# Performance work log

Measured on AMD Instinct MI355X. Metric: run time of the kernel, lower is better.

## Reference

```python
import jax, jax.numpy as jnp
import numpy as np

LN_EPS = 1e-5
BN_EPS = 1e-5
ATTN_EPS = 1e-6

def _ln(x, g, b):
    m = x.mean(-1, keepdims=True)
    v = x.var(-1, keepdims=True)
    return (x - m) / jnp.sqrt(v + LN_EPS) * g + b

def setup_inputs() -> dict:
    key = jax.random.key(0)
    ks = jax.random.split(key, 16)
    B, C, N = 4, 256, 8192
    s = 0.05
    def rn(k, shape, scale=1.0):
        return jax.random.normal(k, shape, jnp.float32) * scale
    return {
        "x1": rn(ks[0], (B, C, N)),
        "x2": rn(ks[1], (B, C, N)),
        "Wq": rn(ks[2], (C, C), s), "bq": rn(ks[3], (C,), s),
        "Wk": rn(ks[4], (C, C), s), "bk": rn(ks[5], (C,), s),
        "Wv": rn(ks[6], (C, C), s), "bv": rn(ks[7], (C,), s),
        "threshold": jnp.array([0.1], jnp.float32),
        "W1": rn(ks[8], (2 * C, 2 * C), s),
        "W2": rn(ks[9], (C, 2 * C), s),
        "g1": jnp.ones((C,), jnp.float32), "b1": jnp.zeros((C,), jnp.float32),
        "g2": jnp.ones((C,), jnp.float32), "b2": jnp.zeros((C,), jnp.float32),
        "Wa": rn(ks[10], (C, C), s), "ba": rn(ks[11], (C,), s),
        "bn_g": jnp.ones((C,), jnp.float32), "bn_b": jnp.zeros((C,), jnp.float32),
        "bn_m": jnp.zeros((C,), jnp.float32), "bn_v": jnp.ones((C,), jnp.float32),
    }

def reference(x1, x2, Wq, bq, Wk, bk, Wv, bv, threshold, W1, W2,
              g1, b1, g2, b2, Wa, ba, bn_g, bn_b, bn_m, bn_v):
    B, C, N = x1.shape
    H = 4
    d = C // H
    def conv1x1(x, W, b):  # nn.Conv1d(C, C, 1): [B,C,N] -> [B,C,N]
        return jnp.einsum('bcn,oc->bon', x, W) + b[:, None]
    # projections -> [B, N, H, d]
    q = conv1x1(x1, Wq, bq).transpose(0, 2, 1).reshape(B, N, H, d)
    k = conv1x1(x2, Wk, bk).transpose(0, 2, 1).reshape(B, N, H, d)
    v = conv1x1(x2, Wv, bv).transpose(0, 2, 1).reshape(B, N, H, d)
    # DynamicSparseLinearAttention
    Q = jax.nn.elu(q) + 1.0
    K = jax.nn.elu(k) + 1.0
    S = v.shape[1]
    vals = v / S
    KV = jnp.einsum('nshd,nshv->nhdv', K, vals)               # [B,H,d,d]
    scores = jnp.einsum('nlhd,nhd->nlh', Q, K.sum(axis=1))    # [B,N,H]
    sparse = jnp.where(scores > threshold[0], scores, 0.0)
    Z = 1.0 / (sparse + ATTN_EPS)
    msg = jnp.einsum('nlhd,nhdv,nlh->nlhv', Q, KV, Z) * S     # [B,N,H,d]
    # view [B,N,C]; the transpose(1,2).transpose(1,2) in torch cancels
    msg = msg.reshape(B, N, H * d)
    msg = _ln(msg, g1, b1)
    msg = jnp.concatenate([x1.transpose(0, 2, 1), msg], axis=2)  # [B,N,2C]
    msg = jax.nn.relu(msg @ W1.T) @ W2.T                         # [B,N,C]
    msg = _ln(msg, g2, b2).transpose(0, 2, 1)                    # [B,C,N]
    # aug shortcut: conv1x1 + BatchNorm1d (eval mode, running stats)
    aug = conv1x1(x1, Wa, ba)
    aug = (aug - bn_m[None, :, None]) / jnp.sqrt(bn_v[None, :, None] + BN_EPS)
    aug = aug * bn_g[None, :, None] + bn_b[None, :, None]
    return msg + x1 + aug
```

## Files before the change

kernel.cpp:

```cpp
#include <hip/hip_runtime.h>

#define BB 4
#define CC 256
#define NN 8192
#define HH 4
#define NCH 16

typedef unsigned short u16;
typedef __bf16 bf16x8 __attribute__((ext_vector_type(8)));
typedef float f32x4 __attribute__((ext_vector_type(4)));

__device__ __forceinline__ float bf2f(unsigned u) {
  return __uint_as_float(u << 16);
}
__device__ __forceinline__ u16 f2bf(float f) {
  unsigned u = __float_as_uint(f);
  return (u16)((u + 0x7fffu + ((u >> 16) & 1u)) >> 16);
}
__device__ __forceinline__ void bf8_to_f32(uint4 r, float* f) {
  f[0] = __uint_as_float(r.x << 16); f[1] = __uint_as_float(r.x & 0xffff0000u);
  f[2] = __uint_as_float(r.y << 16); f[3] = __uint_as_float(r.y & 0xffff0000u);
  f[4] = __uint_as_float(r.z << 16); f[5] = __uint_as_float(r.z & 0xffff0000u);
  f[6] = __uint_as_float(r.w << 16); f[7] = __uint_as_float(r.w & 0xffff0000u);
}

__global__ __launch_bounds__(256) void cvt_all_kernel(
    const float* __restrict__ wq, const float* __restrict__ wk,
    const float* __restrict__ wv, const float* __restrict__ wa,
    const float* __restrict__ w1, const float* __restrict__ w2,
    u16* __restrict__ oq, u16* __restrict__ ok, u16* __restrict__ ov,
    u16* __restrict__ oa, u16* __restrict__ o1, u16* __restrict__ o2) {
  int i = blockIdx.x * 256 + threadIdx.x;
  const float* src;
  u16* dst;
  int off;
  if (i < 65536) { src = wq; dst = oq; off = i; }
  else if (i < 131072) { src = wk; dst = ok; off = i - 65536; }
  else if (i < 196608) { src = wv; dst = ov; off = i - 131072; }
  else if (i < 262144) { src = wa; dst = oa; off = i - 196608; }
  else if (i < 524288) { src = w1; dst = o1; off = i - 262144; }
  else { src = w2; dst = o2; off = i - 524288; }
  dst[off] = f2bf(src[off]);
}

__global__ __launch_bounds__(256) void transpose_kernel(const float* __restrict__ x1,
                                                        const float* __restrict__ x2,
                                                        u16* __restrict__ x1t,
                                                        u16* __restrict__ x2t) {
  __shared__ float T[64][65];
  const int bz = blockIdx.z;
  const int b = bz & 3;
  const float* x = (bz < 4) ? x1 : x2;
  u16* xt = (bz < 4) ? x1t : x2t;
  const int c0 = blockIdx.y * 64, n0 = blockIdx.x * 64;
  const float* xp = x + ((size_t)b * CC + c0) * NN + n0;
#pragma unroll
  for (int it = 0; it < 4; ++it) {
    int idx = threadIdx.x + it * 256;
    int r = idx >> 4, seg = idx & 15;
    float4 v = *(const float4*)(xp + (size_t)r * NN + seg * 4);
    T[r][seg * 4 + 0] = v.x; T[r][seg * 4 + 1] = v.y;
    T[r][seg * 4 + 2] = v.z; T[r][seg * 4 + 3] = v.w;
  }
  __syncthreads();
  u16* op = xt + ((size_t)b * NN + n0) * CC + c0;
  const int j = threadIdx.x >> 2, g = threadIdx.x & 3;
#pragma unroll
  for (int i = 0; i < 4; ++i) {
    int c = g * 16 + i * 4;
    uint2 pk;
    pk.x = (unsigned)f2bf(T[c + 0][j]) | ((unsigned)f2bf(T[c + 1][j]) << 16);
    pk.y = (unsigned)f2bf(T[c + 2][j]) | ((unsigned)f2bf(T[c + 3][j]) << 16);
    *(uint2*)(op + (size_t)j * CC + c) = pk;
  }
}

template <int MODE>
__global__ __launch_bounds__(256) void gemm_kernel(
    const u16* __restrict__ A1, const u16* __restrict__ A2,
    const u16* __restrict__ W, const float* __restrict__ bias,
    const float* __restrict__ e0, const float* __restrict__ e1,
    const float* __restrict__ e2, const float* __restrict__ e3,
    u16* __restrict__ outp, int K, int O) {
  __shared__ u16 As[128][72];
  __shared__ u16 Ws[128][72];
  const int m0 = blockIdx.x * 128, o0 = blockIdx.y * 128;
  const int tid = threadIdx.x, lane = tid & 63, wave = tid >> 6;
  const int wm = (wave >> 1) * 64, wo = (wave & 1) * 64;
  const int fr = lane & 15, fq = lane >> 4;
  f32x4 acc[4][4] = {};
  const int nkt = K >> 6;
  for (int kt = 0; kt < nkt; ++kt) {
    const int k0 = kt << 6;
    const u16* Ap;
    int rsA;
    if (MODE == 4) {
      Ap = (k0 < 256) ? (A1 + k0) : (A2 + (k0 - 256));
      rsA = 256;
    } else {
      Ap = A1 + k0;
      rsA = K;
    }
    const u16* Wp = W + k0;
#pragma unroll
    for (int i = 0; i < 4; ++i) {
      int idx = tid + i * 256;
      int r = idx >> 3, s = idx & 7;
      *(uint4*)(&As[r][s * 8]) = *(const uint4*)(Ap + (size_t)(m0 + r) * rsA + s * 8);
      *(uint4*)(&Ws[r][s * 8]) = *(const uint4*)(Wp + (size_t)(o0 + r) * K + s * 8);
    }
    __syncthreads();
#pragma unroll
    for (int kk = 0; kk < 2; ++kk) {
      bf16x8 af[4], bfr[4];
#pragma unroll
      for (int mi = 0; mi < 4; ++mi)
        af[mi] = __builtin_bit_cast(bf16x8, *(const uint4*)(&As[wm + mi * 16 + fr][kk * 32 + fq * 8]));
#pragma unroll
      for (int oi = 0; oi < 4; ++oi)
        bfr[oi] = __builtin_bit_cast(bf16x8, *(const uint4*)(&Ws[wo + oi * 16 + fr][kk * 32 + fq * 8]));
#pragma unroll
      for (int mi = 0; mi < 4; ++mi)
#pragma unroll
        for (int oi = 0; oi < 4; ++oi)
          acc[mi][oi] = __builtin_amdgcn_mfma_f32_16x16x32_bf16(af[mi], bfr[oi], acc[mi][oi], 0, 0, 0);
    }
    __syncthreads();
  }
  const int bb_ = m0 >> 13;
  const int nb = m0 & (NN - 1);
#pragma unroll
  for (int oi = 0; oi < 4; ++oi) {
    const int col = o0 + wo + oi * 16 + fr;
    float b0 = 0.f, sc = 1.f, sh = 0.f;
    if (MODE == 0 || MODE == 1 || MODE == 2) b0 = bias[col];
    if (MODE == 3) {
      sc = e0[col] * rsqrtf(e3[col] + 1e-5f);
      sh = (bias[col] - e2[col]) * sc + e1[col];
    }
#pragma unroll
    for (int mi = 0; mi < 4; ++mi) {
      const int rowb = m0 + wm + mi * 16 + fq * 4;
      if (MODE == 1 || MODE == 2) {
        float v[4];
#pragma unroll
        for (int r = 0; r < 4; ++r) {
          float t = acc[mi][oi][r] + b0;
          if (MODE == 1) t = (t > 0.f) ? (t + 1.f) : __expf(t);
          v[r] = t;
        }
        uint2 pk;
        pk.x = (unsigned)f2bf(v[0]) | ((unsigned)f2bf(v[1]) << 16);
        pk.y = (unsigned)f2bf(v[2]) | ((unsigned)f2bf(v[3]) << 16);
        const int nloc = nb + wm + mi * 16 + fq * 4;
        *(uint2*)(outp + ((size_t)bb_ * CC + col) * NN + nloc) = pk;
      } else {
#pragma unroll
        for (int r = 0; r < 4; ++r) {
          float v = acc[mi][oi][r];
          if (MODE == 0) {
            v += b0;
            v = (v > 0.f) ? (v + 1.f) : __expf(v);
          } else if (MODE == 3) {
            v = v * sc + sh;
          } else if (MODE == 4) {
            v = fmaxf(v, 0.f);
          }
          outp[(size_t)(rowb + r) * O + col] = f2bf(v);
        }
      }
    }
  }
}

__global__ __launch_bounds__(256) void ksum_kernel(const u16* __restrict__ K2,
                                                   float* __restrict__ Ksum) {
  __shared__ float red[4];
  const int b = blockIdx.y, c = blockIdx.x, tid = threadIdx.x;
  const u16* p = K2 + ((size_t)b * CC + c) * NN;
  float acc = 0.f;
#pragma unroll
  for (int j = 0; j < 4; ++j) {
    uint4 raw = *(const uint4*)(p + (j * 256 + tid) * 8);
    float f[8];
    bf8_to_f32(raw, f);
#pragma unroll
    for (int q = 0; q < 8; ++q) acc += f[q];
  }
#pragma unroll
  for (int m = 1; m < 64; m <<= 1) acc += __shfl_xor(acc, m);
  if ((tid & 63) == 0) red[tid >> 6] = acc;
  __syncthreads();
  if (tid == 0) Ksum[b * CC + c] = red[0] + red[1] + red[2] + red[3];
}

__global__ __launch_bounds__(256) void kvpartial_kernel(const u16* __restrict__ K2,
                                                        const u16* __restrict__ V2,
                                                        float* __restrict__ Pkv) {
  __shared__ u16 Ks[64][72];
  __shared__ u16 Vs[64][72];
  const int b = blockIdx.z, h = blockIdx.y, ch = blockIdx.x;
  const int tid = threadIdx.x, lane = tid & 63, w = tid >> 6;
  const int fr = lane & 15, fq = lane >> 4;
  const size_t base = ((size_t)b * CC + h * 64) * NN + (size_t)ch * (NN / NCH);
  f32x4 acc[4] = {};
  for (int step = 0; step < (NN / NCH) / 64; ++step) {
#pragma unroll
    for (int i = 0; i < 2; ++i) {
      int r = (tid >> 3) + i * 32, s = tid & 7;
      *(uint4*)(&Ks[r][s * 8]) = *(const uint4*)(K2 + base + (size_t)r * NN + step * 64 + s * 8);
      *(uint4*)(&Vs[r][s * 8]) = *(const uint4*)(V2 + base + (size_t)r * NN + step * 64 + s * 8);
    }
    __syncthreads();
#pragma unroll
    for (int kk = 0; kk < 2; ++kk) {
      bf16x8 af = __builtin_bit_cast(bf16x8, *(const uint4*)(&Ks[w * 16 + fr][kk * 32 + fq * 8]));
#pragma unroll
      for (int oi = 0; oi < 4; ++oi) {
        bf16x8 bfr = __builtin_bit_cast(bf16x8, *(const uint4*)(&Vs[oi * 16 + fr][kk * 32 + fq * 8]));
        acc[oi] = __builtin_amdgcn_mfma_f32_16x16x32_bf16(af, bfr, acc[oi], 0, 0, 0);
      }
    }
    __syncthreads();
  }
  float* o = Pkv + (((size_t)ch * (BB * HH) + b * HH + h) << 12);
#pragma unroll
  for (int oi = 0; oi < 4; ++oi)
#pragma unroll
    for (int r = 0; r < 4; ++r)
      o[(w * 16 + fq * 4 + r) * 64 + oi * 16 + fr] = acc[oi][r];
}

__global__ __launch_bounds__(256) void kvreduce_kernel(const float* __restrict__ Pkv,
                                                       u16* __restrict__ KVT) {
  int i = blockIdx.x * 256 + threadIdx.x;
  int bh = i >> 12, dk = (i >> 6) & 63, dv = i & 63;
  float s = 0.f;
#pragma unroll
  for (int ch = 0; ch < NCH; ++ch)
    s += Pkv[(((size_t)ch * (BB * HH) + bh) << 12) + (dk << 6) + dv];
  KVT[((size_t)bh << 12) + (dv << 6) + dk] = f2bf(s);
}

__global__ __launch_bounds__(256) void score_kernel(const u16* __restrict__ Qt,
                                                    const float* __restrict__ Ksum,
                                                    const float* __restrict__ thrp,
                                                    float* __restrict__ Zbuf) {
  int gid = blockIdx.x * 256 + threadIdx.x;
  int b = gid >> 13;
  const u16* qp = Qt + (size_t)gid * CC;
  const float* ks = Ksum + b * CC;
  float acc[HH] = {0.f, 0.f, 0.f, 0.f};
  for (int c8 = 0; c8 < 32; ++c8) {
    uint4 raw = *(const uint4*)(qp + c8 * 8);
    float f[8];
    bf8_to_f32(raw, f);
    float s = 0.f;
#pragma unroll
    for (int j = 0; j < 8; ++j) s += f[j] * ks[c8 * 8 + j];
    acc[c8 >> 3] += s;
  }
  float thr = thrp[0];
  float4 z;
  z.x = 1.f / (((acc[0] > thr) ? acc[0] : 0.f) + 1e-6f);
  z.y = 1.f / (((acc[1] > thr) ? acc[1] : 0.f) + 1e-6f);
  z.z = 1.f / (((acc[2] > thr) ? acc[2] : 0.f) + 1e-6f);
  z.w = 1.f / (((acc[3] > thr) ? acc[3] : 0.f) + 1e-6f);
  *(float4*)(Zbuf + (size_t)gid * 4) = z;
}

__global__ __launch_bounds__(256) void msggemm_kernel(const u16* __restrict__ Qt,
                                                      const u16* __restrict__ KVT,
                                                      const float* __restrict__ Zbuf,
                                                      u16* __restrict__ msgout) {
  __shared__ u16 As[128][72];
  __shared__ u16 Ws[64][72];
  const int m0 = blockIdx.x * 128, h = blockIdx.y, b = blockIdx.z;
  const int tid = threadIdx.x, lane = tid & 63, wave = tid >> 6;
  const int wm = (wave >> 1) * 64, wo = (wave & 1) * 32;
  const int fr = lane & 15, fq = lane >> 4;
  const u16* Ap = Qt + ((size_t)b * NN + m0) * CC + h * 64;
#pragma unroll
  for (int i = 0; i < 4; ++i) {
    int idx = tid + i * 256;
    int r = idx >> 3, s = idx & 7;
    *(uint4*)(&As[r][s * 8]) = *(const uint4*)(Ap + (size_t)r * CC + s * 8);
  }
  const u16* Wp = KVT + (((size_t)b * HH + h) << 12);
#pragma unroll
  for (int i = 0; i < 2; ++i) {
    int idx = tid + i * 256;
    int r = idx >> 3, s = idx & 7;
    *(uint4*)(&Ws[r][s * 8]) = *(const uint4*)(Wp + (size_t)r * 64 + s * 8);
  }
  __syncthreads();
  f32x4 acc[4][2] = {};
#pragma unroll
  for (int kk = 0; kk < 2; ++kk) {
    bf16x8 af[4], bfr[2];
#pragma unroll
    for (int mi = 0; mi < 4; ++mi)
      af[mi] = __builtin_bit_cast(bf16x8, *(const uint4*)(&As[wm + mi * 16 + fr][kk * 32 + fq * 8]));
#pragma unroll
    for (int oi = 0; oi < 2; ++oi)
      bfr[oi] = __builtin_bit_cast(bf16x8, *(const uint4*)(&Ws[wo + oi * 16 + fr][kk * 32 + fq * 8]));
#pragma unroll
    for (int mi = 0; mi < 4; ++mi)
#pragma unroll
      for (int oi = 0; oi < 2; ++oi)
        acc[mi][oi] = __builtin_amdgcn_mfma_f32_16x16x32_bf16(af[mi], bfr[oi], acc[mi][oi], 0, 0, 0);
  }
#pragma unroll
  for (int oi = 0; oi < 2; ++oi) {
    const int col = h * 64 + wo + oi * 16 + fr;
#pragma unroll
    for (int mi = 0; mi < 4; ++mi) {
      const int rowb = m0 + wm + mi * 16 + fq * 4;
#pragma unroll
      for (int r = 0; r < 4; ++r) {
        const int row = rowb + r;
        float z = Zbuf[((size_t)b * NN + row) * HH + h];
        msgout[((size_t)b * NN + row) * CC + col] = f2bf(acc[mi][oi][r] * z);
      }
    }
  }
}

template <bool AUG>
__global__ __launch_bounds__(256) void ln_kernel(const u16* __restrict__ in,
                                                 u16* __restrict__ outb,
                                                 const float* __restrict__ g,
                                                 const float* __restrict__ bb,
                                                 const u16* __restrict__ aug) {
  const int tid = threadIdx.x, lane = tid & 63, w = tid >> 6;
  const size_t row0 = (size_t)blockIdx.x * 32;
  float gv[4], bv[4];
#pragma unroll
  for (int q = 0; q < 4; ++q) {
    gv[q] = g[lane + 64 * q];
    bv[q] = bb[lane + 64 * q];
  }
  for (int i = 0; i < 8; ++i) {
    const size_t row = row0 + i * 4 + w;
    const u16* p = in + row * CC;
    float v[4], s1 = 0.f, s2 = 0.f;
#pragma unroll
    for (int q = 0; q < 4; ++q) {
      v[q] = bf2f(p[lane + 64 * q]);
      s1 += v[q];
      s2 += v[q] * v[q];
    }
#pragma unroll
    for (int m = 1; m < 64; m <<= 1) {
      s1 += __shfl_xor(s1, m);
      s2 += __shfl_xor(s2, m);
    }
    const float mean = s1 * (1.f / CC);
    const float var = s2 * (1.f / CC) - mean * mean;
    const float rs = rsqrtf(var + 1e-5f);
    u16* o = outb + row * CC;
#pragma unroll
    for (int q = 0; q < 4; ++q) {
      float ov = (v[q] - mean) * rs * gv[q] + bv[q];
      if (AUG) ov += bf2f(aug[row * CC + lane + 64 * q]);
      o[lane + 64 * q] = f2bf(ov);
    }
  }
}

__global__ __launch_bounds__(256) void addout_kernel(const u16* __restrict__ tv,
                                                     const float* __restrict__ x1,
                                                     float* __restrict__ outp) {
  __shared__ float T[64][65];
  const int b = blockIdx.z, c0 = blockIdx.y * 64, n0 = blockIdx.x * 64;
  const u16* tp = tv + ((size_t)b * NN + n0) * CC + c0;
#pragma unroll
  for (int i = 0; i < 2; ++i) {
    int idx = threadIdx.x + i * 256;
    int r = idx >> 3, s = idx & 7;
    uint4 raw = *(const uint4*)(tp + (size_t)r * CC + s * 8);
    float f[8];
    bf8_to_f32(raw, f);
#pragma unroll
    for (int j = 0; j < 8; ++j) T[s * 8 + j][r] = f[j];
  }
  __syncthreads();
  const float* xp = x1 + ((size_t)b * CC + c0) * NN + n0;
  float* op = outp + ((size_t)b * CC + c0) * NN + n0;
#pragma unroll
  for (int i = 0; i < 16; ++i) {
    int idx = threadIdx.x + i * 256;
    int c = idx >> 6, j = idx & 63;
    op[(size_t)c * NN + j] = T[c][j] + xp[(size_t)c * NN + j];
  }
}

extern "C" void kernel_launch(void* const* d_in, const int* in_sizes, int n_in,
                              void* d_out, int out_size, void* d_ws, size_t ws_size,
                              hipStream_t stream) {
  (void)in_sizes; (void)n_in; (void)out_size; (void)ws_size;
  const float* x1 = (const float*)d_in[0];
  const float* x2 = (const float*)d_in[1];
  const float* Wq = (const float*)d_in[2];
  const float* bq = (const float*)d_in[3];
  const float* Wk = (const float*)d_in[4];
  const float* bk = (const float*)d_in[5];
  const float* Wv = (const float*)d_in[6];
  const float* bv = (const float*)d_in[7];
  const float* thr = (const float*)d_in[8];
  const float* W1 = (const float*)d_in[9];
  const float* W2 = (const float*)d_in[10];
  const float* g1 = (const float*)d_in[11];
  const float* b1 = (const float*)d_in[12];
  const float* g2 = (const float*)d_in[13];
  const float* b2 = (const float*)d_in[14];
  const float* Wa = (const float*)d_in[15];
  const float* ba = (const float*)d_in[16];
  const float* bng = (const float*)d_in[17];
  const float* bnb = (const float*)d_in[18];
  const float* bnm = (const float*)d_in[19];
  const float* bnv = (const float*)d_in[20];
  float* out = (float*)d_out;

  char* ws = (char*)d_ws;
  constexpr size_t SZ = (size_t)BB * NN * CC * sizeof(u16);
  u16* x1t = (u16*)(ws);
  u16* x2t = (u16*)(ws + SZ);
  u16* Qt = (u16*)(ws + 2 * SZ);
  u16* K2 = (u16*)(ws + 3 * SZ);
  u16* V2 = (u16*)(ws + 4 * SZ);
  u16* augt = (u16*)(ws + 5 * SZ);
  u16* msgout = (u16*)(ws + 6 * SZ);
  u16* h1 = Qt;
  u16* mlp2 = x2t;
  u16* msgN = V2;
  u16* tv = V2;
  float* Pkv = (float*)msgout;
  char* tail = ws + 7 * SZ;
  float* Ksum = (float*)tail;
  float* Zbuf = (float*)(tail + 4096);
  u16* KVT = (u16*)(tail + 4096 + 524288);
  u16* Wqb = (u16*)(tail + 4096 + 524288 + 131072);
  u16* Wkb = Wqb + CC * CC;
  u16* Wvb = Wkb + CC * CC;
  u16* Wab = Wvb + CC * CC;
  u16* W1b = Wab + CC * CC;
  u16* W2b = W1b + 512 * 512;

  cvt_all_kernel<<<dim3(2560), 256, 0, stream>>>(Wq, Wk, Wv, Wa, W1, W2,
                                                 Wqb, Wkb, Wvb, Wab, W1b, W2b);

  transpose_kernel<<<dim3(NN / 64, CC / 64, 2 * BB), 256, 0, stream>>>(x1, x2, x1t, x2t);

  gemm_kernel<0><<<dim3(256, 2), 256, 0, stream>>>(x1t, nullptr, Wqb, bq, nullptr, nullptr, nullptr, nullptr, Qt, 256, 256);
  gemm_kernel<1><<<dim3(256, 2), 256, 0, stream>>>(x2t, nullptr, Wkb, bk, nullptr, nullptr, nullptr, nullptr, K2, 256, 256);
  gemm_kernel<2><<<dim3(256, 2), 256, 0, stream>>>(x2t, nullptr, Wvb, bv, nullptr, nullptr, nullptr, nullptr, V2, 256, 256);
  gemm_kernel<3><<<dim3(256, 2), 256, 0, stream>>>(x1t, nullptr, Wab, ba, bng, bnb, bnm, bnv, augt, 256, 256);

  ksum_kernel<<<dim3(CC, BB), 256, 0, stream>>>(K2, Ksum);
  kvpartial_kernel<<<dim3(NCH, HH, BB), 256, 0, stream>>>(K2, V2, Pkv);
  kvreduce_kernel<<<dim3(256), 256, 0, stream>>>(Pkv, KVT);
  score_kernel<<<dim3(128), 256, 0, stream>>>(Qt, Ksum, thr, Zbuf);
  msggemm_kernel<<<dim3(NN / 128, HH, BB), 256, 0, stream>>>(Qt, KVT, Zbuf, msgout);
  ln_kernel<false><<<dim3(1024), 256, 0, stream>>>(msgout, msgN, g1, b1, nullptr);

  gemm_kernel<4><<<dim3(256, 4), 256, 0, stream>>>(x1t, msgN, W1b, nullptr, nullptr, nullptr, nullptr, nullptr, h1, 512, 512);
  gemm_kernel<5><<<dim3(256, 2), 256, 0, stream>>>(h1, nullptr, W2b, nullptr, nullptr, nullptr, nullptr, nullptr, mlp2, 512, 256);

  ln_kernel<true><<<dim3(1024), 256, 0, stream>>>(mlp2, tv, g2, b2, augt);
  addout_kernel<<<dim3(NN / 64, CC / 64, BB), 256, 0, stream>>>(tv, x1, out);
}
```

Measured before the change: 187.5 us.

## Use direct global-to-LDS loads, fuse score into msggemm, vectorize layernorm

GEMM and KV-partial tiles are now loaded straight from global memory into LDS with global_load_lds, and the padded LDS rows are dropped so the direct-load layout fits. The score/Z computation moves into the message GEMM, which computes it from the Q tile already staged in LDS, removing one launch and the Zbuf round trip. LayerNorm now reads and writes four contiguous bf16 values per lane instead of strided scalar accesses. Removing the row padding may bring back LDS bank conflicts on the MFMA fragment reads.

Measured after the change: 192.1 us. 2.4% more time.

```diff
diff --git a/kernel.cpp b/kernel.cpp
--- a/kernel.cpp
+++ b/kernel.cpp
@@ -22,6 +22,15 @@
   f[2] = __uint_as_float(r.y << 16); f[3] = __uint_as_float(r.y & 0xffff0000u);
   f[4] = __uint_as_float(r.z << 16); f[5] = __uint_as_float(r.z & 0xffff0000u);
   f[6] = __uint_as_float(r.w << 16); f[7] = __uint_as_float(r.w & 0xffff0000u);
+}
+__device__ __forceinline__ void bf4_to_f32(uint2 r, float* f) {
+  f[0] = __uint_as_float(r.x << 16); f[1] = __uint_as_float(r.x & 0xffff0000u);
+  f[2] = __uint_as_float(r.y << 16); f[3] = __uint_as_float(r.y & 0xffff0000u);
+}
+__device__ __forceinline__ void gload16(const u16* g, u16* l) {
+  __builtin_amdgcn_global_load_lds(
+      (const __attribute__((address_space(1))) unsigned int*)g,
+      (__attribute__((address_space(3))) unsigned int*)l, 16, 0, 0);
 }
 
 __global__ __launch_bounds__(256) void cvt_all_kernel(
@@ -82,8 +91,8 @@
     const float* __restrict__ e0, const float* __restrict__ e1,
     const float* __restrict__ e2, const float* __restrict__ e3,
     u16* __restrict__ outp, int K, int O) {
-  __shared__ u16 As[128][72];
-  __shared__ u16 Ws[128][72];
+  __shared__ u16 As[128 * 64];
+  __shared__ u16 Ws[128 * 64];
   const int m0 = blockIdx.x * 128, o0 = blockIdx.y * 128;
   const int tid = threadIdx.x, lane = tid & 63, wave = tid >> 6;
   const int wm = (wave >> 1) * 64, wo = (wave & 1) * 64;
@@ -105,9 +114,9 @@
 #pragma unroll
     for (int i = 0; i < 4; ++i) {
       int idx = tid + i * 256;
-      int r = idx >> 3, s = idx & 7;
-      *(uint4*)(&As[r][s * 8]) = *(const uint4*)(Ap + (size_t)(m0 + r) * rsA + s * 8);
-      *(uint4*)(&Ws[r][s * 8]) = *(const uint4*)(Wp + (size_t)(o0 + r) * K + s * 8);
+      int rr = idx >> 3, ss = idx & 7;
+      gload16(Ap + (size_t)(m0 + rr) * rsA + ss * 8, &As[(i * 256 + wave * 64) * 8]);
+      gload16(Wp + (size_t)(o0 + rr) * K + ss * 8, &Ws[(i * 256 + wave * 64) * 8]);
     }
     __syncthreads();
 #pragma unroll
@@ -115,10 +124,10 @@
       bf16x8 af[4], bfr[4];
 #pragma unroll
       for (int mi = 0; mi < 4; ++mi)
-        af[mi] = __builtin_bit_cast(bf16x8, *(const uint4*)(&As[wm + mi * 16 + fr][kk * 32 + fq * 8]));
+        af[mi] = __builtin_bit_cast(bf16x8, *(const uint4*)(&As[(wm + mi * 16 + fr) * 64 + kk * 32 + fq * 8]));
 #pragma unroll
       for (int oi = 0; oi < 4; ++oi)
-        bfr[oi] = __builtin_bit_cast(bf16x8, *(const uint4*)(&Ws[wo + oi * 16 + fr][kk * 32 + fq * 8]));
+        bfr[oi] = __builtin_bit_cast(bf16x8, *(const uint4*)(&Ws[(wo + oi * 16 + fr) * 64 + kk * 32 + fq * 8]));
 #pragma unroll
       for (int mi = 0; mi < 4; ++mi)
 #pragma unroll
@@ -197,8 +206,8 @@
 __global__ __launch_bounds__(256) void kvpartial_kernel(const u16* __restrict__ K2,
                                                         const u16* __restrict__ V2,
                                                         float* __restrict__ Pkv) {
-  __shared__ u16 Ks[64][72];
-  __shared__ u16 Vs[64][72];
+  __shared__ u16 Ks[64 * 64];
+  __shared__ u16 Vs[64 * 64];
   const int b = blockIdx.z, h = blockIdx.y, ch = blockIdx.x;
   const int tid = threadIdx.x, lane = tid & 63, w = tid >> 6;
   const int fr = lane & 15, fq = lane >> 4;
@@ -207,17 +216,18 @@
   for (int step = 0; step < (NN / NCH) / 64; ++step) {
 #pragma unroll
     for (int i = 0; i < 2; ++i) {
-      int r = (tid >> 3) + i * 32, s = tid & 7;
-      *(uint4*)(&Ks[r][s * 8]) = *(const uint4*)(K2 + base + (size_t)r * NN + step * 64 + s * 8);
-      *(uint4*)(&Vs[r][s * 8]) = *(const uint4*)(V2 + base + (size_t)r * NN + step * 64 + s * 8);
+      int idx = tid + i * 256;
+      int rr = idx >> 3, ss = idx & 7;
+      gload16(K2 + base + (size_t)rr * NN + step * 64 + ss * 8, &Ks[(i * 256 + w * 64) * 8]);
+      gload16(V2 + base + (size_t)rr * NN + step * 64 + ss * 8, &Vs[(i * 256 + w * 64) * 8]);
     }
     __syncthreads();
 #pragma unroll
     for (int kk = 0; kk < 2; ++kk) {
-      bf16x8 af = __builtin_bit_cast(bf16x8, *(const uint4*)(&Ks[w * 16 + fr][kk * 32 + fq * 8]));
+      bf16x8 af = __builtin_bit_cast(bf16x8, *(const uint4*)(&Ks[(w * 16 + fr) * 64 + kk * 32 + fq * 8]));
 #pragma unroll
       for (int oi = 0; oi < 4; ++oi) {
-        bf16x8 bfr = __builtin_bit_cast(bf16x8, *(const uint4*)(&Vs[oi * 16 + fr][kk * 32 + fq * 8]));
+        bf16x8 bfr = __builtin_bit_cast(bf16x8, *(const uint4*)(&Vs[(oi * 16 + fr) * 64 + kk * 32 + fq * 8]));
         acc[oi] = __builtin_amdgcn_mfma_f32_16x16x32_bf16(af, bfr, acc[oi], 0, 0, 0);
       }
     }
@@ -242,85 +252,76 @@
   KVT[((size_t)bh << 12) + (dv << 6) + dk] = f2bf(s);
 }
 
-__global__ __launch_bounds__(256) void score_kernel(const u16* __restrict__ Qt,
-                                                    const float* __restrict__ Ksum,
-                                                    const float* __restrict__ thrp,
-                                                    float* __restrict__ Zbuf) {
-  int gid = blockIdx.x * 256 + threadIdx.x;
-  int b = gid >> 13;
-  const u16* qp = Qt + (size_t)gid * CC;
-  const float* ks = Ksum + b * CC;
-  float acc[HH] = {0.f, 0.f, 0.f, 0.f};
-  for (int c8 = 0; c8 < 32; ++c8) {
-    uint4 raw = *(const uint4*)(qp + c8 * 8);
-    float f[8];
-    bf8_to_f32(raw, f);
-    float s = 0.f;
-#pragma unroll
-    for (int j = 0; j < 8; ++j) s += f[j] * ks[c8 * 8 + j];
-    acc[c8 >> 3] += s;
-  }
-  float thr = thrp[0];
-  float4 z;
-  z.x = 1.f / (((acc[0] > thr) ? acc[0] : 0.f) + 1e-6f);
-  z.y = 1.f / (((acc[1] > thr) ? acc[1] : 0.f) + 1e-6f);
-  z.z = 1.f / (((acc[2] > thr) ? acc[2] : 0.f) + 1e-6f);
-  z.w = 1.f / (((acc[3] > thr) ? acc[3] : 0.f) + 1e-6f);
-  *(float4*)(Zbuf + (size_t)gid * 4) = z;
-}
-
 __global__ __launch_bounds__(256) void msggemm_kernel(const u16* __restrict__ Qt,
                                                       const u16* __restrict__ KVT,
-                                                      const float* __restrict__ Zbuf,
+                                                      const float* __restrict__ Ksum,
+                                                      const float* __restrict__ thrp,
                                                       u16* __restrict__ msgout) {
-  __shared__ u16 As[128][72];
-  __shared__ u16 Ws[64][72];
+  __shared__ u16 As[128 * 64];
+  __shared__ u16 Ws[64 * 64];
+  __shared__ float Zs[128];
   const int m0 = blockIdx.x * 128, h = blockIdx.y, b = blockIdx.z;
   const int tid = threadIdx.x, lane = tid & 63, wave = tid >> 6;
   const int wm = (wave >> 1) * 64, wo = (wave & 1) * 32;
   const int fr = lane & 15, fq = lane >> 4;
+  const float thrv = thrp[0];
   const u16* Ap = Qt + ((size_t)b * NN + m0) * CC + h * 64;
 #pragma unroll
   for (int i = 0; i < 4; ++i) {
     int idx = tid + i * 256;
-    int r = idx >> 3, s = idx & 7;
-    *(uint4*)(&As[r][s * 8]) = *(const uint4*)(Ap + (size_t)r * CC + s * 8);
+    int rr = idx >> 3, ss = idx & 7;
+    gload16(Ap + (size_t)rr * CC + ss * 8, &As[(i * 256 + wave * 64) * 8]);
   }
   const u16* Wp = KVT + (((size_t)b * HH + h) << 12);
 #pragma unroll
   for (int i = 0; i < 2; ++i) {
     int idx = tid + i * 256;
-    int r = idx >> 3, s = idx & 7;
-    *(uint4*)(&Ws[r][s * 8]) = *(const uint4*)(Wp + (size_t)r * 64 + s * 8);
+    int rr = idx >> 3, ss = idx & 7;
+    gload16(Wp + (size_t)rr * 64 + ss * 8, &Ws[(i * 256 + wave * 64) * 8]);
   }
   __syncthreads();
+  {
+    const int row = tid >> 1, half = tid & 1;
+    const float* ksh = Ksum + b * CC + h * 64 + half * 32;
+    float za = 0.f;
+#pragma unroll
+    for (int j8 = 0; j8 < 4; ++j8) {
+      uint4 raw = *(const uint4*)(&As[row * 64 + half * 32 + j8 * 8]);
+      float f[8];
+      bf8_to_f32(raw, f);
+#pragma unroll
+      for (int j = 0; j < 8; ++j) za += f[j] * ksh[j8 * 8 + j];
+    }
+    za += __shfl_xor(za, 1);
+    if (half == 0) Zs[row] = 1.f / (((za > thrv) ? za : 0.f) + 1e-6f);
+  }
   f32x4 acc[4][2] = {};
 #pragma unroll
   for (int kk = 0; kk < 2; ++kk) {
     bf16x8 af[4], bfr[2];
 #pragma unroll
     for (int mi = 0; mi < 4; ++mi)
-      af[mi] = __builtin_bit_cast(bf16x8, *(const uint4*)(&As[wm + mi * 16 + fr][kk * 32 + fq * 8]));
+      af[mi] = __builtin_bit_cast(bf16x8, *(const uint4*)(&As[(wm + mi * 16 + fr) * 64 + kk * 32 + fq * 8]));
 #pragma unroll
     for (int oi = 0; oi < 2; ++oi)
-      bfr[oi] = __builtin_bit_cast(bf16x8, *(const uint4*)(&Ws[wo + oi * 16 + fr][kk * 32 + fq * 8]));
+      bfr[oi] = __builtin_bit_cast(bf16x8, *(const uint4*)(&Ws[(wo + oi * 16 + fr) * 64 + kk * 32 + fq * 8]));
 #pragma unroll
     for (int mi = 0; mi < 4; ++mi)
 #pragma unroll
       for (int oi = 0; oi < 2; ++oi)
         acc[mi][oi] = __builtin_amdgcn_mfma_f32_16x16x32_bf16(af[mi], bfr[oi], acc[mi][oi], 0, 0, 0);
   }
+  __syncthreads();
 #pragma unroll
   for (int oi = 0; oi < 2; ++oi) {
     const int col = h * 64 + wo + oi * 16 + fr;
 #pragma unroll
     for (int mi = 0; mi < 4; ++mi) {
-      const int rowb = m0 + wm + mi * 16 + fq * 4;
+      const int rowb = wm + mi * 16 + fq * 4;
 #pragma unroll
       for (int r = 0; r < 4; ++r) {
         const int row = rowb + r;
-        float z = Zbuf[((size_t)b * NN + row) * HH + h];
-        msgout[((size_t)b * NN + row) * CC + col] = f2bf(acc[mi][oi][r] * z);
+        msgout[((size_t)b * NN + m0 + row) * CC + col] = f2bf(acc[mi][oi][r] * Zs[row]);
       }
     }
   }
@@ -337,19 +338,16 @@
   float gv[4], bv[4];
 #pragma unroll
   for (int q = 0; q < 4; ++q) {
-    gv[q] = g[lane + 64 * q];
-    bv[q] = bb[lane + 64 * q];
+    gv[q] = g[lane * 4 + q];
+    bv[q] = bb[lane * 4 + q];
   }
   for (int i = 0; i < 8; ++i) {
     const size_t row = row0 + i * 4 + w;
-    const u16* p = in + row * CC;
-    float v[4], s1 = 0.f, s2 = 0.f;
-#pragma unroll
-    for (int q = 0; q < 4; ++q) {
-      v[q] = bf2f(p[lane + 64 * q]);
-      s1 += v[q];
-      s2 += v[q] * v[q];
-    }
+    uint2 raw = *(const uint2*)(in + row * CC + lane * 4);
+    float v[4];
+    bf4_to_f32(raw, v);
+    float s1 = v[0] + v[1] + v[2] + v[3];
+    float s2 = v[0] * v[0] + v[1] * v[1] + v[2] * v[2] + v[3] * v[3];
 #pragma unroll
     for (int m = 1; m < 64; m <<= 1) {
       s1 += __shfl_xor(s1, m);
@@ -358,13 +356,20 @@
     const float mean = s1 * (1.f / CC);
     const float var = s2 * (1.f / CC) - mean * mean;
     const float rs = rsqrtf(var + 1e-5f);
-    u16* o = outb + row * CC;
-#pragma unroll
-    for (int q = 0; q < 4; ++q) {
-      float ov = (v[q] - mean) * rs * gv[q] + bv[q];
-      if (AUG) ov += bf2f(aug[row * CC + lane + 64 * q]);
-      o[lane + 64 * q] = f2bf(ov);
-    }
+    float ov[4];
+#pragma unroll
+    for (int q = 0; q < 4; ++q) ov[q] = (v[q] - mean) * rs * gv[q] + bv[q];
+    if (AUG) {
+      uint2 ar = *(const uint2*)(aug + row * CC + lane * 4);
+      float af[4];
+      bf4_to_f32(ar, af);
+#pragma unroll
+      for (int q = 0; q < 4; ++q) ov[q] += af[q];
+    }
+    uint2 pk;
+    pk.x = (unsigned)f2bf(ov[0]) | ((unsigned)f2bf(ov[1]) << 16);
+    pk.y = (unsigned)f2bf(ov[2]) | ((unsigned)f2bf(ov[3]) << 16);
+    *(uint2*)(outb + row * CC + lane * 4) = pk;
   }
 }
 
@@ -438,9 +443,8 @@
   float* Pkv = (float*)msgout;
   char* tail = ws + 7 * SZ;
   float* Ksum = (float*)tail;
-  float* Zbuf = (float*)(tail + 4096);
-  u16* KVT = (u16*)(tail + 4096 + 524288);
-  u16* Wqb = (u16*)(tail + 4096 + 524288 + 131072);
+  u16* KVT = (u16*)(tail + 4096);
+  u16* Wqb = (u16*)(tail + 4096 + 131072);
   u16* Wkb = Wqb + CC * CC;
   u16* Wvb = Wkb + CC * CC;
   u16* Wab = Wvb + CC * CC;
@@ -460,8 +464,7 @@
   ksum_kernel<<<dim3(CC, BB), 256, 0, stream>>>(K2, Ksum);
   kvpartial_kernel<<<dim3(NCH, HH, BB), 256, 0, stream>>>(K2, V2, Pkv);
   kvreduce_kernel<<<dim3(256), 256, 0, stream>>>(Pkv, KVT);
-  score_kernel<<<dim3(128), 256, 0, stream>>>(Qt, Ksum, thr, Zbuf);
-  msggemm_kernel<<<dim3(NN / 128, HH, BB), 256, 0, stream>>>(Qt, KVT, Zbuf, msgout);
+  msggemm_kernel<<<dim3(NN / 128, HH, BB), 256, 0, stream>>>(Qt, KVT, Ksum, thr, msgout);
   ln_kernel<false><<<dim3(1024), 256, 0, stream>>>(msgout, msgN, g1, b1, nullptr);
 
   gemm_kernel<4><<<dim3(256, 4), 256, 0, stream>>>(x1t, msgN, W1b, nullptr, nullptr, nullptr, nullptr, nullptr, h1, 512, 512);
```
